# Performance work log

Measured on AMD Instinct MI355X. Metric: run time of the kernel, lower is better.

The kernel has to match this reference:

```python
import jax, jax.numpy as jnp
import numpy as np

N, E = 50000, 800000
F_IN, H, OUT, L = 32, 128, 20, 4


def setup_inputs() -> dict:
    key = jax.random.key(0)
    ks = jax.random.split(key, 32)
    s = 0.05  # weight scale
    inp = {
        "h": jax.random.normal(ks[0], (N, F_IN), jnp.float32),
        "x": jax.random.normal(ks[1], (N, 3), jnp.float32),
        "edges": jax.random.randint(ks[2], (2, E), 0, N, jnp.int32),
        # embeddings
        "emb_in_w": jax.random.normal(ks[3], (F_IN, H)) * s,
        "emb_in_b": jnp.zeros((H,)),
        "emb_out_w": jax.random.normal(ks[4], (H, H)) * s,
        "emb_out_b": jnp.zeros((H,)),
        # per-layer stacked params
        "edge_w1": jax.random.normal(ks[5], (L, 2 * H + 1, H)) * s,
        "edge_b1": jnp.zeros((L, H)),
        "edge_w2": jax.random.normal(ks[6], (L, H, H)) * s,
        "edge_b2": jnp.zeros((L, H)),
        "att_w": jax.random.normal(ks[7], (L, H, 1)) * s,
        "att_b": jnp.zeros((L, 1)),
        "coord_w1": jax.random.normal(ks[8], (L, H, H)) * s,
        "coord_b1": jnp.zeros((L, H)),
        "coord_w2": jax.random.normal(ks[9], (L, H, 1)) * s,  # no bias (egnn_clean)
        "node_w1": jax.random.normal(ks[10], (L, 2 * H, H)) * s,
        "node_b1": jnp.zeros((L, H)),
        "node_w2": jax.random.normal(ks[11], (L, H, H)) * s,
        "node_b2": jnp.zeros((L, H)),
        # head MLP
        "head_w1": jax.random.normal(ks[12], (H, H)) * s,
        "head_b1": jnp.zeros((H,)),
        "head_w2": jax.random.normal(ks[13], (H, OUT)) * s,
        "head_b2": jnp.zeros((OUT,)),
    }
    return inp


def reference(h, x, edges, emb_in_w, emb_in_b, emb_out_w, emb_out_b,
              edge_w1, edge_b1, edge_w2, edge_b2, att_w, att_b,
              coord_w1, coord_b1, coord_w2,
              node_w1, node_b1, node_w2, node_b2,
              head_w1, head_b1, head_w2, head_b2):
    n = h.shape[0]
    row, col = edges[0], edges[1]
    h = h @ emb_in_w + emb_in_b
    for l in range(L):
        diff = x[row] - x[col]                       # [E,3]
        radial = jnp.sum(diff * diff, -1, keepdims=True)  # [E,1]
        m = jnp.concatenate([h[row], h[col], radial], -1)  # [E,2H+1]
        m = jax.nn.silu(m @ edge_w1[l] + edge_b1[l])
        m = jax.nn.silu(m @ edge_w2[l] + edge_b2[l])
        m = m * jax.nn.sigmoid(m @ att_w[l] + att_b[l])  # attention gate
        # coordinate update: segment mean of diff * coord_mlp(m)
        cw = jax.nn.silu(m @ coord_w1[l] + coord_b1[l]) @ coord_w2[l]  # [E,1]
        trans = diff * cw
        agg_x = jax.ops.segment_sum(trans, row, num_segments=n)
        cnt = jax.ops.segment_sum(jnp.ones((E, 1), trans.dtype), row, num_segments=n)
        x = x + agg_x / jnp.maximum(cnt, 1.0)
        # node update: residual MLP on [h, segment_sum(m)]
        agg_m = jax.ops.segment_sum(m, row, num_segments=n)
        hcat = jnp.concatenate([h, agg_m], -1)
        h = h + (jax.nn.silu(hcat @ node_w1[l] + node_b1[l]) @ node_w2[l] + node_b2[l])
    h = h @ emb_out_w + emb_out_b
    g = jnp.mean(h, axis=0)  # mean pool over nodes
    out = jax.nn.relu(g @ head_w1 + head_b1) @ head_w2 + head_b2
    return out[None, :]  # [1, OUT]
```

## Files before the change

### kernel.cpp

```cpp
#include <hip/hip_runtime.h>
#include <hip/hip_bf16.h>

#define NN   50000
#define EE   800000
#define FIN  32
#define HH   128
#define LL   4
#define NOUT 20
#define EPB  128
#define ETHR 512

typedef __attribute__((ext_vector_type(8))) short bf16x8;
typedef __attribute__((ext_vector_type(4))) short short4v;
typedef __attribute__((ext_vector_type(4))) float f32x4;

__device__ __forceinline__ float silu_f(float v){ return v / (1.f + __expf(-v)); }
__device__ __forceinline__ float sigm_f(float v){ return 1.f / (1.f + __expf(-v)); }

__device__ __forceinline__ short f2bf(float v){
  union { float f; unsigned u; } a; a.f = v;
  unsigned r = a.u + 0x7fff + ((a.u >> 16) & 1);
  return (short)(r >> 16);
}
__device__ __forceinline__ float bf2f(short s){
  union { unsigned u; float f; } a; a.u = ((unsigned)(unsigned short)s) << 16;
  return a.f;
}

__device__ __forceinline__ f32x4 mfma16(bf16x8 a, bf16x8 b, f32x4 c){
  return __builtin_amdgcn_mfma_f32_16x16x32_bf16(a, b, c, 0, 0, 0);
}

__device__ __forceinline__ void gemm8(const short* Ah, const short* Al,
                                      const short* __restrict__ Wh,
                                      const short* __restrict__ Wl,
                                      int cl, int g, int wc0, f32x4 acc[8])
{
  const int wb = (wc0 + cl)*HH + g*8;
  #pragma unroll
  for (int kb = 0; kb < 4; kb++) {
    const int kk = kb*32 + g*8;
    const bf16x8 bh = *(const bf16x8*)&Wh[wb + kb*32];
    const bf16x8 bl = *(const bf16x8*)&Wl[wb + kb*32];
    #pragma unroll
    for (int fr = 0; fr < 8; fr++) {
      const int e = fr*16 + cl;
      const int off = e*128 + (kk ^ ((e&7)<<3));
      const bf16x8 ah = *(const bf16x8*)&Ah[off];
      const bf16x8 al = *(const bf16x8*)&Al[off];
      acc[fr] = mfma16(ah, bh, acc[fr]);
      acc[fr] = mfma16(ah, bl, acc[fr]);
      acc[fr] = mfma16(al, bh, acc[fr]);
    }
  }
}

__global__ __launch_bounds__(256)
void k_prep(const float* __restrict__ ew1, const float* __restrict__ ew2,
            const float* __restrict__ cw1v, short* __restrict__ wph,
            short* __restrict__ wpl)
{
  const int b = blockIdx.x;
  const int l = b >> 2, m = b & 3;
  const float* src = (m==0) ? ew1 + (size_t)l*(2*HH+1)*HH
                   : (m==1) ? ew1 + (size_t)l*(2*HH+1)*HH + HH*HH
                   : (m==2) ? ew2 + (size_t)l*HH*HH
                            : cw1v + (size_t)l*HH*HH;
  short* dh = wph + (size_t)b*HH*HH;
  short* dl = wpl + (size_t)b*HH*HH;
  for (int idx = threadIdx.x; idx < HH*HH; idx += 256) {
    const int k = idx >> 7, c = idx & 127;
    const float v = src[idx];
    const short hh = f2bf(v);
    dh[c*HH + k] = hh;
    dl[c*HH + k] = f2bf(v - bf2f(hh));
  }
}

__global__ __launch_bounds__(256)
void k_embed(const float* __restrict__ hin, const float* __restrict__ xin,
             const float* __restrict__ W, const float* __restrict__ b,
             float* __restrict__ hout, float* __restrict__ xout,
             short* __restrict__ hbi, short* __restrict__ hlo)
{
  __shared__ float wl[FIN*HH];
  const int tid = threadIdx.x;
  for (int j = tid; j < FIN*HH; j += 256) wl[j] = W[j];
  __syncthreads();
  const int c  = tid & (HH-1);
  const int no = tid >> 7;
  const int v  = blockIdx.x * 2 + no;
  if (v < NN) {
    const float* hr = hin + (size_t)v * FIN;
    float acc = b[c];
    #pragma unroll
    for (int k = 0; k < FIN; k++) acc = fmaf(hr[k], wl[k*HH + c], acc);
    hout[(size_t)v*HH + c] = acc;
    const short hh = f2bf(acc);
    hbi[(size_t)v*HH + c] = hh;
    hlo[(size_t)v*HH + c] = f2bf(acc - bf2f(hh));
    if (c < 3) xout[v*3 + c] = xin[v*3 + c];
  }
}

__global__ __launch_bounds__(256)
void k_count(const int* __restrict__ row, int* __restrict__ deg)
{
  const int e = blockIdx.x * 256 + threadIdx.x;
  if (e < EE) atomicAdd(&deg[row[e]], 1);
}

__global__ __launch_bounds__(1024)
void k_scan(const int* __restrict__ deg, int* __restrict__ offs, int* __restrict__ cursor)
{
  __shared__ int part[1024];
  const int t = threadIdx.x;
  const int base = t * 49;
  int s = 0;
  for (int i = 0; i < 49; i++) { const int idx = base + i; s += (idx < NN) ? deg[idx] : 0; }
  part[t] = s;
  __syncthreads();
  if (t == 0) { int run = 0; for (int i = 0; i < 1024; i++) { const int v = part[i]; part[i] = run; run += v; } }
  __syncthreads();
  int run = part[t];
  for (int i = 0; i < 49; i++) {
    const int idx = base + i;
    if (idx < NN) { offs[idx] = run; cursor[idx] = run; run += deg[idx]; }
  }
  if (t == 1023) offs[NN] = EE;
}

__global__ __launch_bounds__(256)
void k_pos(const int* __restrict__ row, int* __restrict__ cursor, int* __restrict__ pos)
{
  const int e = blockIdx.x * 256 + threadIdx.x;
  if (e < EE) pos[e] = atomicAdd(&cursor[row[e]], 1);
}

template<bool SC>
__global__ __launch_bounds__(ETHR, 4)
void k_edge(const short* __restrict__ hbi, const short* __restrict__ hlo,
            const float* __restrict__ xbuf,
            const int* __restrict__ row, const int* __restrict__ col,
            const int* __restrict__ pos,
            const short* __restrict__ wph, const short* __restrict__ wpl, int lidx,
            const float* __restrict__ W1, const float* __restrict__ b1,
            const float* __restrict__ b2,
            const float* __restrict__ attw, const float* __restrict__ attb,
            const float* __restrict__ cb1, const float* __restrict__ cw2,
            float* __restrict__ mbuf, float* __restrict__ aggx)
{
  __shared__ short Ah[EPB*128];
  __shared__ short Al[EPB*128];
  __shared__ float red[8][EPB];
  __shared__ float scal[EPB];
  __shared__ int   rowb[EPB];
  __shared__ int   colb[EPB];
  __shared__ int   posb[EPB];
  __shared__ float diffb[EPB][3];
  __shared__ float radb[EPB];

  const int tid  = threadIdx.x;
  const int lane = tid & 63;
  const int wv   = tid >> 6;
  const int cl   = lane & 15;
  const int g    = lane >> 4;
  const int wc0  = wv * 16;
  const int col0 = wc0 + cl;
  const int eb   = blockIdx.x * EPB;

  const short* W1a_h = wph + (size_t)(lidx*4+0)*HH*HH;
  const short* W1a_l = wpl + (size_t)(lidx*4+0)*HH*HH;
  const short* W1b_h = wph + (size_t)(lidx*4+1)*HH*HH;
  const short* W1b_l = wpl + (size_t)(lidx*4+1)*HH*HH;
  const short* W2_h  = wph + (size_t)(lidx*4+2)*HH*HH;
  const short* W2_l  = wpl + (size_t)(lidx*4+2)*HH*HH;
  const short* C1_h  = wph + (size_t)(lidx*4+3)*HH*HH;
  const short* C1_l  = wpl + (size_t)(lidx*4+3)*HH*HH;

  if (tid < EPB) {
    const int r  = row[eb + tid];
    const int c2 = col[eb + tid];
    rowb[tid] = r; colb[tid] = c2;
    if (SC) posb[tid] = pos[eb + tid];
    const float dx = xbuf[r*3+0] - xbuf[c2*3+0];
    const float dy = xbuf[r*3+1] - xbuf[c2*3+1];
    const float dz = xbuf[r*3+2] - xbuf[c2*3+2];
    diffb[tid][0] = dx; diffb[tid][1] = dy; diffb[tid][2] = dz;
    radb[tid] = dx*dx + dy*dy + dz*dz;
  }
  __syncthreads();

  const int se = tid >> 2;
  const int sq = tid & 3;
  {
    const int base = rowb[se]*HH;
    #pragma unroll
    for (int u = 0; u < 4; u++) {
      const int c = sq*8 + u*32;
      const int o = se*128 + (c ^ ((se&7)<<3));
      *(bf16x8*)&Ah[o] = *(const bf16x8*)&hbi[base + c];
      *(bf16x8*)&Al[o] = *(const bf16x8*)&hlo[base + c];
    }
  }
  bf16x8 pch[4], pcl[4];
  {
    const int base = colb[se]*HH;
    #pragma unroll
    for (int u = 0; u < 4; u++) {
      const int c = sq*8 + u*32;
      pch[u] = *(const bf16x8*)&hbi[base + c];
      pcl[u] = *(const bf16x8*)&hlo[base + c];
    }
  }
  __syncthreads();

  f32x4 acc[8];
  #pragma unroll
  for (int fr = 0; fr < 8; fr++) acc[fr] = (f32x4){0,0,0,0};
  gemm8(Ah, Al, W1a_h, W1a_l, cl, g, wc0, acc);
  __syncthreads();

  {
    #pragma unroll
    for (int u = 0; u < 4; u++) {
      const int c = sq*8 + u*32;
      const int o = se*128 + (c ^ ((se&7)<<3));
      *(bf16x8*)&Ah[o] = pch[u];
      *(bf16x8*)&Al[o] = pcl[u];
    }
  }
  __syncthreads();

  gemm8(Ah, Al, W1b_h, W1b_l, cl, g, wc0, acc);
  {
    const float w256 = W1[(size_t)(2*HH)*HH + col0];
    const float bb   = b1[col0];
    #pragma unroll
    for (int fr = 0; fr < 8; fr++) {
      #pragma unroll
      for (int j = 0; j < 4; j++) {
        const int r = fr*16 + g*4 + j;
        acc[fr][j] = silu_f(fmaf(radb[r], w256, acc[fr][j]) + bb);
      }
    }
  }
  __syncthreads();

  #pragma unroll
  for (int fr = 0; fr < 8; fr++) {
    #pragma unroll
    for (int j = 0; j < 4; j++) {
      const int r = fr*16 + g*4 + j;
      const int sw = (r&7)<<3;
      const float v = acc[fr][j];
      const short h0 = f2bf(v);
      Ah[r*128 + (col0 ^ sw)] = h0;
      Al[r*128 + (col0 ^ sw)] = f2bf(v - bf2f(h0));
    }
  }
  __syncthreads();

  f32x4 m2[8];
  #pragma unroll
  for (int fr = 0; fr < 8; fr++) m2[fr] = (f32x4){0,0,0,0};
  gemm8(Ah, Al, W2_h, W2_l, cl, g, wc0, m2);
  {
    const float bb = b2[col0];
    const float aw = attw[col0];
    #pragma unroll
    for (int fr = 0; fr < 8; fr++) {
      #pragma unroll
      for (int j = 0; j < 4; j++) {
        m2[fr][j] = silu_f(m2[fr][j] + bb);
        float p = m2[fr][j] * aw;
        p += __shfl_xor(p, 1); p += __shfl_xor(p, 2);
        p += __shfl_xor(p, 4); p += __shfl_xor(p, 8);
        if (cl == 0) red[wv][fr*16 + g*4 + j] = p;
      }
    }
  }
  __syncthreads();

  if (tid < EPB) {
    float s = attb[0];
    #pragma unroll
    for (int w = 0; w < 8; w++) s += red[w][tid];
    scal[tid] = sigm_f(s);
  }
  __syncthreads();

  #pragma unroll
  for (int fr = 0; fr < 8; fr++) {
    #pragma unroll
    for (int j = 0; j < 4; j++) {
      const int r = fr*16 + g*4 + j;
      const float v = m2[fr][j] * scal[r];
      if (SC) {
        mbuf[(size_t)posb[r]*HH + col0] = v;
      } else {
        atomicAdd(&mbuf[(size_t)rowb[r]*HH + col0], v);
      }
      const int sw = (r&7)<<3;
      const short h0 = f2bf(v);
      Ah[r*128 + (col0 ^ sw)] = h0;
      Al[r*128 + (col0 ^ sw)] = f2bf(v - bf2f(h0));
    }
  }
  __syncthreads();

  f32x4 a3[8];
  #pragma unroll
  for (int fr = 0; fr < 8; fr++) a3[fr] = (f32x4){0,0,0,0};
  gemm8(Ah, Al, C1_h, C1_l, cl, g, wc0, a3);
  {
    const float bb = cb1[col0];
    const float c2 = cw2[col0];
    #pragma unroll
    for (int fr = 0; fr < 8; fr++) {
      #pragma unroll
      for (int j = 0; j < 4; j++) {
        float p = silu_f(a3[fr][j] + bb) * c2;
        p += __shfl_xor(p, 1); p += __shfl_xor(p, 2);
        p += __shfl_xor(p, 4); p += __shfl_xor(p, 8);
        if (cl == 0) red[wv][fr*16 + g*4 + j] = p;
      }
    }
  }
  __syncthreads();

  if (tid < EPB) {
    float cwv = 0.f;
    #pragma unroll
    for (int w = 0; w < 8; w++) cwv += red[w][tid];
    const int r = rowb[tid];
    atomicAdd(&aggx[r*3+0], diffb[tid][0]*cwv);
    atomicAdd(&aggx[r*3+1], diffb[tid][1]*cwv);
    atomicAdd(&aggx[r*3+2], diffb[tid][2]*cwv);
  }
}

__device__ __forceinline__ void gemm_accum(const float (*buf)[132], const float* __restrict__ W,
                                           int c, int eo, float acc[32])
{
  for (int k0 = 0; k0 < HH; k0 += 4) {
    const float w0 = W[(k0+0)*HH + c];
    const float w1 = W[(k0+1)*HH + c];
    const float w2 = W[(k0+2)*HH + c];
    const float w3 = W[(k0+3)*HH + c];
    #pragma unroll
    for (int i = 0; i < 32; i++) {
      const float4 a = *(const float4*)&buf[eo*32+i][k0];
      acc[i] = fmaf(a.x, w0, fmaf(a.y, w1, fmaf(a.z, w2, fmaf(a.w, w3, acc[i]))));
    }
  }
}

template<bool SC>
__global__ __launch_bounds__(256, 2)
void k_node(float* __restrict__ hbuf, float* __restrict__ xbuf,
            const float* __restrict__ mbuf, const int* __restrict__ offs,
            const float* __restrict__ aggx,
            const float* __restrict__ W1, const float* __restrict__ b1,
            const float* __restrict__ W2, const float* __restrict__ b2,
            short* __restrict__ hbi, short* __restrict__ hlo)
{
  __shared__ float bufA[64][132];
  __shared__ float bufB[64][132];
  const int tid = threadIdx.x;
  const int c   = tid & (HH-1);
  const int no  = tid >> 7;
  const int nb  = blockIdx.x * 64;

  #pragma unroll
  for (int i = 0; i < 32; i++) {
    const int v = nb + no*32 + i;
    bufA[no*32+i][c] = (v < NN) ? hbuf[(size_t)v*HH + c] : 0.f;
  }
  __syncthreads();

  float acc[32];
  #pragma unroll
  for (int i = 0; i < 32; i++) acc[i] = 0.f;
  gemm_accum(bufA, W1, c, no, acc);
  __syncthreads();

  for (int i = 0; i < 32; i++) {
    const int v = nb + no*32 + i;
    float s = 0.f;
    if (v < NN) {
      if (SC) {
        const int beg = offs[v], end = offs[v+1];
        for (int j = beg; j < end; j++) s += mbuf[(size_t)j*HH + c];
      } else {
        s = mbuf[(size_t)v*HH + c];
      }
    }
    bufA[no*32+i][c] = s;
  }
  __syncthreads();
  gemm_accum(bufA, W1 + HH*HH, c, no, acc);
  {
    const float bb = b1[c];
    #pragma unroll
    for (int i = 0; i < 32; i++) bufB[no*32+i][c] = silu_f(acc[i] + bb);
  }
  __syncthreads();

  #pragma unroll
  for (int i = 0; i < 32; i++) acc[i] = 0.f;
  gemm_accum(bufB, W2, c, no, acc);
  {
    const float bb = b2[c];
    #pragma unroll
    for (int i = 0; i < 32; i++) {
      const int v = nb + no*32 + i;
      if (v < NN) {
        const float hn = hbuf[(size_t)v*HH + c] + acc[i] + bb;
        hbuf[(size_t)v*HH + c] = hn;
        const short hh = f2bf(hn);
        hbi[(size_t)v*HH + c] = hh;
        hlo[(size_t)v*HH + c] = f2bf(hn - bf2f(hh));
      }
    }
  }

  if (tid < 64) {
    const int v = nb + tid;
    if (v < NN) {
      const float ct = fmaxf((float)(offs[v+1] - offs[v]), 1.f);
      xbuf[v*3+0] += aggx[v*3+0] / ct;
      xbuf[v*3+1] += aggx[v*3+1] / ct;
      xbuf[v*3+2] += aggx[v*3+2] / ct;
    }
  }
}

__global__ __launch_bounds__(128)
void k_pool(const float* __restrict__ h, float* __restrict__ g)
{
  const int c  = threadIdx.x;
  const int v0 = blockIdx.x * 100;
  float s = 0.f;
  for (int v = v0; v < v0 + 100; ++v) s += h[(size_t)v*HH + c];
  atomicAdd(&g[c], s);
}

__global__ __launch_bounds__(128)
void k_head(const float* __restrict__ g,
            const float* __restrict__ eow, const float* __restrict__ eob,
            const float* __restrict__ hw1, const float* __restrict__ hb1,
            const float* __restrict__ hw2, const float* __restrict__ hb2,
            float* __restrict__ out)
{
  __shared__ float gm[HH], ho[HH], t1[HH];
  const int c = threadIdx.x;
  gm[c] = g[c] * (1.f / (float)NN);
  __syncthreads();
  float a = eob[c];
  for (int k = 0; k < HH; k++) a = fmaf(gm[k], eow[k*HH + c], a);
  ho[c] = a;
  __syncthreads();
  float t = hb1[c];
  for (int k = 0; k < HH; k++) t = fmaf(ho[k], hw1[k*HH + c], t);
  t1[c] = fmaxf(t, 0.f);
  __syncthreads();
  if (c < NOUT) {
    float o = hb2[c];
    for (int k = 0; k < HH; k++) o = fmaf(t1[k], hw2[k*NOUT + c], o);
    out[c] = o;
  }
}

extern "C" void kernel_launch(void* const* d_in, const int* in_sizes, int n_in,
                              void* d_out, int out_size, void* d_ws, size_t ws_size,
                              hipStream_t stream)
{
  const float* in_h  = (const float*)d_in[0];
  const float* in_x  = (const float*)d_in[1];
  const int*   edges = (const int*)  d_in[2];
  const float* eiw   = (const float*)d_in[3];
  const float* eib   = (const float*)d_in[4];
  const float* eow   = (const float*)d_in[5];
  const float* eob   = (const float*)d_in[6];
  const float* ew1   = (const float*)d_in[7];
  const float* eb1   = (const float*)d_in[8];
  const float* ew2   = (const float*)d_in[9];
  const float* eb2   = (const float*)d_in[10];
  const float* attw  = (const float*)d_in[11];
  const float* attb  = (const float*)d_in[12];
  const float* cw1   = (const float*)d_in[13];
  const float* cb1   = (const float*)d_in[14];
  const float* cw2   = (const float*)d_in[15];
  const float* nw1   = (const float*)d_in[16];
  const float* nb1   = (const float*)d_in[17];
  const float* nw2   = (const float*)d_in[18];
  const float* nb2   = (const float*)d_in[19];
  const float* hw1   = (const float*)d_in[20];
  const float* hb1   = (const float*)d_in[21];
  const float* hw2   = (const float*)d_in[22];
  const float* hb2   = (const float*)d_in[23];

  const int* row = edges;
  const int* col = edges + EE;

  char* p = (char*)d_ws;
  auto alloc = [&](size_t bytes) { char* r = p; p += (bytes + 255) & ~(size_t)255; return r; };
  float* h    = (float*)alloc((size_t)NN*HH*4);
  float* x    = (float*)alloc((size_t)NN*3*4);
  float* aggx = (float*)alloc((size_t)NN*3*4);
  float* g    = (float*)alloc(HH*4);
  int*   deg  = (int*)  alloc((size_t)NN*4);
  int*   offs = (int*)  alloc((size_t)(NN+1)*4);
  int*   curs = (int*)  alloc((size_t)NN*4);
  int*   pos  = (int*)  alloc((size_t)EE*4);
  short* hbi  = (short*)alloc((size_t)NN*HH*2);
  short* hlo  = (short*)alloc((size_t)NN*HH*2);
  short* wph  = (short*)alloc((size_t)16*HH*HH*2);
  short* wpl  = (short*)alloc((size_t)16*HH*HH*2);
  const size_t baseUsed = (size_t)(p - (char*)d_ws);
  const bool sc = (ws_size >= baseUsed + (size_t)EE*HH*4);
  float* mbuf = (float*)alloc(sc ? (size_t)EE*HH*4 : (size_t)NN*HH*4);

  k_prep<<<16, 256, 0, stream>>>(ew1, ew2, cw1, wph, wpl);
  k_embed<<<NN/2, 256, 0, stream>>>(in_h, in_x, eiw, eib, h, x, hbi, hlo);

  hipMemsetAsync(deg, 0, (size_t)NN*4, stream);
  k_count<<<(EE+255)/256, 256, 0, stream>>>(row, deg);
  k_scan<<<1, 1024, 0, stream>>>(deg, offs, curs);
  k_pos<<<(EE+255)/256, 256, 0, stream>>>(row, curs, pos);

  for (int l = 0; l < LL; l++) {
    hipMemsetAsync(aggx, 0, (size_t)NN*3*4, stream);
    if (!sc) hipMemsetAsync(mbuf, 0, (size_t)NN*HH*4, stream);
    if (sc) {
      k_edge<true><<<EE/EPB, ETHR, 0, stream>>>(hbi, hlo, x, row, col, pos,
          wph, wpl, l,
          ew1 + (size_t)l*(2*HH+1)*HH, eb1 + l*HH, eb2 + l*HH,
          attw + l*HH, attb + l, cb1 + l*HH, cw2 + l*HH,
          mbuf, aggx);
      k_node<true><<<(NN + 63)/64, 256, 0, stream>>>(h, x, mbuf, offs, aggx,
          nw1 + (size_t)l*(2*HH)*HH, nb1 + l*HH,
          nw2 + (size_t)l*HH*HH,     nb2 + l*HH, hbi, hlo);
    } else {
      k_edge<false><<<EE/EPB, ETHR, 0, stream>>>(hbi, hlo, x, row, col, pos,
          wph, wpl, l,
          ew1 + (size_t)l*(2*HH+1)*HH, eb1 + l*HH, eb2 + l*HH,
          attw + l*HH, attb + l, cb1 + l*HH, cw2 + l*HH,
          mbuf, aggx);
      k_node<false><<<(NN + 63)/64, 256, 0, stream>>>(h, x, mbuf, offs, aggx,
          nw1 + (size_t)l*(2*HH)*HH, nb1 + l*HH,
          nw2 + (size_t)l*HH*HH,     nb2 + l*HH, hbi, hlo);
    }
  }

  hipMemsetAsync(g, 0, HH*4, stream);
  k_pool<<<500, 128, 0, stream>>>(h, g);
  k_head<<<1, 128, 0, stream>>>(g, eow, eob, hw1, hb1, hw2, hb2, (float*)d_out);
}
```

Measured before the change: 3.771 ms.

## Retile edge-kernel MFMA warps into 2x4 edge-by-column fragments

Each of the 8 warps in the edge kernel previously computed all 128 edges for one 16-column slice, which meant reloading every A fragment from LDS once per warp. Warps now own a 32-edge by 64-column tile (2x4 MFMA fragments), so each A fragment read from LDS feeds four column fragments and the W fragments are loaded once per k-step. This cuts LDS read traffic per MFMA. The attention and coordinate reductions now reduce partly in registers and combine two partials instead of eight, in exchange for more accumulator and B-fragment registers per thread.

```diff
diff --git a/kernel.cpp b/kernel.cpp
--- a/kernel.cpp
+++ b/kernel.cpp
@@ -31,26 +31,34 @@
   return __builtin_amdgcn_mfma_f32_16x16x32_bf16(a, b, c, 0, 0, 0);
 }
 
-__device__ __forceinline__ void gemm8(const short* Ah, const short* Al,
-                                      const short* __restrict__ Wh,
-                                      const short* __restrict__ Wl,
-                                      int cl, int g, int wc0, f32x4 acc[8])
-{
-  const int wb = (wc0 + cl)*HH + g*8;
+__device__ __forceinline__ void gemm24(const short* Ah, const short* Al,
+                                       const short* __restrict__ Wh,
+                                       const short* __restrict__ Wl,
+                                       int cl, int g, int eg, int cg,
+                                       f32x4 acc[2][4])
+{
   #pragma unroll
   for (int kb = 0; kb < 4; kb++) {
     const int kk = kb*32 + g*8;
-    const bf16x8 bh = *(const bf16x8*)&Wh[wb + kb*32];
-    const bf16x8 bl = *(const bf16x8*)&Wl[wb + kb*32];
-    #pragma unroll
-    for (int fr = 0; fr < 8; fr++) {
-      const int e = fr*16 + cl;
+    bf16x8 bh[4], bl[4];
+    #pragma unroll
+    for (int cf = 0; cf < 4; cf++) {
+      const int wb = (cg*64 + cf*16 + cl)*HH + kk;
+      bh[cf] = *(const bf16x8*)&Wh[wb];
+      bl[cf] = *(const bf16x8*)&Wl[wb];
+    }
+    #pragma unroll
+    for (int fr = 0; fr < 2; fr++) {
+      const int e = eg*32 + fr*16 + cl;
       const int off = e*128 + (kk ^ ((e&7)<<3));
       const bf16x8 ah = *(const bf16x8*)&Ah[off];
       const bf16x8 al = *(const bf16x8*)&Al[off];
-      acc[fr] = mfma16(ah, bh, acc[fr]);
-      acc[fr] = mfma16(ah, bl, acc[fr]);
-      acc[fr] = mfma16(al, bh, acc[fr]);
+      #pragma unroll
+      for (int cf = 0; cf < 4; cf++) {
+        acc[fr][cf] = mfma16(ah, bh[cf], acc[fr][cf]);
+        acc[fr][cf] = mfma16(ah, bl[cf], acc[fr][cf]);
+        acc[fr][cf] = mfma16(al, bh[cf], acc[fr][cf]);
+      }
     }
   }
 }
@@ -152,7 +160,7 @@
 {
   __shared__ short Ah[EPB*128];
   __shared__ short Al[EPB*128];
-  __shared__ float red[8][EPB];
+  __shared__ float red[2][EPB];
   __shared__ float scal[EPB];
   __shared__ int   rowb[EPB];
   __shared__ int   colb[EPB];
@@ -165,8 +173,8 @@
   const int wv   = tid >> 6;
   const int cl   = lane & 15;
   const int g    = lane >> 4;
-  const int wc0  = wv * 16;
-  const int col0 = wc0 + cl;
+  const int eg   = wv & 3;
+  const int cg   = wv >> 2;
   const int eb   = blockIdx.x * EPB;
 
   const short* W1a_h = wph + (size_t)(lidx*4+0)*HH*HH;
@@ -215,10 +223,12 @@
   }
   __syncthreads();
 
-  f32x4 acc[8];
-  #pragma unroll
-  for (int fr = 0; fr < 8; fr++) acc[fr] = (f32x4){0,0,0,0};
-  gemm8(Ah, Al, W1a_h, W1a_l, cl, g, wc0, acc);
+  f32x4 acc[2][4];
+  #pragma unroll
+  for (int fr = 0; fr < 2; fr++)
+    #pragma unroll
+    for (int cf = 0; cf < 4; cf++) acc[fr][cf] = (f32x4){0,0,0,0};
+  gemm24(Ah, Al, W1a_h, W1a_l, cl, g, eg, cg, acc);
   __syncthreads();
 
   {
@@ -232,107 +242,132 @@
   }
   __syncthreads();
 
-  gemm8(Ah, Al, W1b_h, W1b_l, cl, g, wc0, acc);
-  {
-    const float w256 = W1[(size_t)(2*HH)*HH + col0];
-    const float bb   = b1[col0];
-    #pragma unroll
-    for (int fr = 0; fr < 8; fr++) {
+  gemm24(Ah, Al, W1b_h, W1b_l, cl, g, eg, cg, acc);
+  {
+    #pragma unroll
+    for (int cf = 0; cf < 4; cf++) {
+      const int c = cg*64 + cf*16 + cl;
+      const float w256 = W1[(size_t)(2*HH)*HH + c];
+      const float bb   = b1[c];
+      #pragma unroll
+      for (int fr = 0; fr < 2; fr++) {
+        #pragma unroll
+        for (int j = 0; j < 4; j++) {
+          const int r = eg*32 + fr*16 + g*4 + j;
+          acc[fr][cf][j] = silu_f(fmaf(radb[r], w256, acc[fr][cf][j]) + bb);
+        }
+      }
+    }
+  }
+  __syncthreads();
+
+  #pragma unroll
+  for (int fr = 0; fr < 2; fr++) {
+    #pragma unroll
+    for (int cf = 0; cf < 4; cf++) {
       #pragma unroll
       for (int j = 0; j < 4; j++) {
-        const int r = fr*16 + g*4 + j;
-        acc[fr][j] = silu_f(fmaf(radb[r], w256, acc[fr][j]) + bb);
-      }
-    }
-  }
-  __syncthreads();
-
-  #pragma unroll
-  for (int fr = 0; fr < 8; fr++) {
-    #pragma unroll
-    for (int j = 0; j < 4; j++) {
-      const int r = fr*16 + g*4 + j;
-      const int sw = (r&7)<<3;
-      const float v = acc[fr][j];
-      const short h0 = f2bf(v);
-      Ah[r*128 + (col0 ^ sw)] = h0;
-      Al[r*128 + (col0 ^ sw)] = f2bf(v - bf2f(h0));
-    }
-  }
-  __syncthreads();
-
-  f32x4 m2[8];
-  #pragma unroll
-  for (int fr = 0; fr < 8; fr++) m2[fr] = (f32x4){0,0,0,0};
-  gemm8(Ah, Al, W2_h, W2_l, cl, g, wc0, m2);
-  {
-    const float bb = b2[col0];
-    const float aw = attw[col0];
-    #pragma unroll
-    for (int fr = 0; fr < 8; fr++) {
+        const int r = eg*32 + fr*16 + g*4 + j;
+        const int c = cg*64 + cf*16 + cl;
+        const int sw = (r&7)<<3;
+        const float v = acc[fr][cf][j];
+        const short h0 = f2bf(v);
+        Ah[r*128 + (c ^ sw)] = h0;
+        Al[r*128 + (c ^ sw)] = f2bf(v - bf2f(h0));
+      }
+    }
+  }
+  __syncthreads();
+
+  f32x4 m2[2][4];
+  #pragma unroll
+  for (int fr = 0; fr < 2; fr++)
+    #pragma unroll
+    for (int cf = 0; cf < 4; cf++) m2[fr][cf] = (f32x4){0,0,0,0};
+  gemm24(Ah, Al, W2_h, W2_l, cl, g, eg, cg, m2);
+  {
+    float bbv[4], awv[4];
+    #pragma unroll
+    for (int cf = 0; cf < 4; cf++) {
+      const int c = cg*64 + cf*16 + cl;
+      bbv[cf] = b2[c]; awv[cf] = attw[c];
+    }
+    #pragma unroll
+    for (int fr = 0; fr < 2; fr++) {
       #pragma unroll
       for (int j = 0; j < 4; j++) {
-        m2[fr][j] = silu_f(m2[fr][j] + bb);
-        float p = m2[fr][j] * aw;
+        float p = 0.f;
+        #pragma unroll
+        for (int cf = 0; cf < 4; cf++) {
+          m2[fr][cf][j] = silu_f(m2[fr][cf][j] + bbv[cf]);
+          p = fmaf(m2[fr][cf][j], awv[cf], p);
+        }
         p += __shfl_xor(p, 1); p += __shfl_xor(p, 2);
         p += __shfl_xor(p, 4); p += __shfl_xor(p, 8);
-        if (cl == 0) red[wv][fr*16 + g*4 + j] = p;
-      }
-    }
-  }
-  __syncthreads();
-
-  if (tid < EPB) {
-    float s = attb[0];
-    #pragma unroll
-    for (int w = 0; w < 8; w++) s += red[w][tid];
-    scal[tid] = sigm_f(s);
-  }
-  __syncthreads();
-
-  #pragma unroll
-  for (int fr = 0; fr < 8; fr++) {
-    #pragma unroll
-    for (int j = 0; j < 4; j++) {
-      const int r = fr*16 + g*4 + j;
-      const float v = m2[fr][j] * scal[r];
-      if (SC) {
-        mbuf[(size_t)posb[r]*HH + col0] = v;
-      } else {
-        atomicAdd(&mbuf[(size_t)rowb[r]*HH + col0], v);
-      }
-      const int sw = (r&7)<<3;
-      const short h0 = f2bf(v);
-      Ah[r*128 + (col0 ^ sw)] = h0;
-      Al[r*128 + (col0 ^ sw)] = f2bf(v - bf2f(h0));
-    }
-  }
-  __syncthreads();
-
-  f32x4 a3[8];
-  #pragma unroll
-  for (int fr = 0; fr < 8; fr++) a3[fr] = (f32x4){0,0,0,0};
-  gemm8(Ah, Al, C1_h, C1_l, cl, g, wc0, a3);
-  {
-    const float bb = cb1[col0];
-    const float c2 = cw2[col0];
-    #pragma unroll
-    for (int fr = 0; fr < 8; fr++) {
+        if (cl == 0) red[cg][eg*32 + fr*16 + g*4 + j] = p;
+      }
+    }
+  }
+  __syncthreads();
+
+  if (tid < EPB)
+    scal[tid] = sigm_f(red[0][tid] + red[1][tid] + attb[0]);
+  __syncthreads();
+
+  #pragma unroll
+  for (int fr = 0; fr < 2; fr++) {
+    #pragma unroll
+    for (int cf = 0; cf < 4; cf++) {
       #pragma unroll
       for (int j = 0; j < 4; j++) {
-        float p = silu_f(a3[fr][j] + bb) * c2;
+        const int r = eg*32 + fr*16 + g*4 + j;
+        const int c = cg*64 + cf*16 + cl;
+        const float v = m2[fr][cf][j] * scal[r];
+        if (SC) {
+          mbuf[(size_t)posb[r]*HH + c] = v;
+        } else {
+          atomicAdd(&mbuf[(size_t)rowb[r]*HH + c], v);
+        }
+        const int sw = (r&7)<<3;
+        const short h0 = f2bf(v);
+        Ah[r*128 + (c ^ sw)] = h0;
+        Al[r*128 + (c ^ sw)] = f2bf(v - bf2f(h0));
+      }
+    }
+  }
+  __syncthreads();
+
+  f32x4 a3[2][4];
+  #pragma unroll
+  for (int fr = 0; fr < 2; fr++)
+    #pragma unroll
+    for (int cf = 0; cf < 4; cf++) a3[fr][cf] = (f32x4){0,0,0,0};
+  gemm24(Ah, Al, C1_h, C1_l, cl, g, eg, cg, a3);
+  {
+    float bbv[4], c2v[4];
+    #pragma unroll
+    for (int cf = 0; cf < 4; cf++) {
+      const int c = cg*64 + cf*16 + cl;
+      bbv[cf] = cb1[c]; c2v[cf] = cw2[c];
+    }
+    #pragma unroll
+    for (int fr = 0; fr < 2; fr++) {
+      #pragma unroll
+      for (int j = 0; j < 4; j++) {
+        float p = 0.f;
+        #pragma unroll
+        for (int cf = 0; cf < 4; cf++)
+          p = fmaf(silu_f(a3[fr][cf][j] + bbv[cf]), c2v[cf], p);
         p += __shfl_xor(p, 1); p += __shfl_xor(p, 2);
         p += __shfl_xor(p, 4); p += __shfl_xor(p, 8);
-        if (cl == 0) red[wv][fr*16 + g*4 + j] = p;
+        if (cl == 0) red[cg][eg*32 + fr*16 + g*4 + j] = p;
       }
     }
   }
   __syncthreads();
 
   if (tid < EPB) {
-    float cwv = 0.f;
-    #pragma unroll
-    for (int w = 0; w < 8; w++) cwv += red[w][tid];
+    const float cwv = red[0][tid] + red[1][tid];
     const int r = rowb[tid];
     atomicAdd(&aggx[r*3+0], diffb[tid][0]*cwv);
     atomicAdd(&aggx[r*3+1], diffb[tid][1]*cwv);
```

Result: slower. 4.933 ms (+30.8%).
